# Kernel optimization log

Measured on AMD Instinct MI355X. Metric: run time of the kernel, lower is better.

## Reference

```python
import jax, jax.numpy as jnp
import numpy as np
from jax import lax

NTAG = 31
HID = 100
NEG = -10000.0


def gru_dir(x, w_ih, w_hh, b_ih, b_hh):
    # x: [T, B, 100]; PyTorch gate order in weights: [r, z, n]
    B = x.shape[1]
    h0 = jnp.zeros((B, HID), dtype=x.dtype)

    def step(h, xt):
        gi = xt @ w_ih.T + b_ih          # [B, 3H]
        gh = h @ w_hh.T + b_hh           # [B, 3H]
        ir, iz, inn = jnp.split(gi, 3, axis=-1)
        hr, hz, hn = jnp.split(gh, 3, axis=-1)
        r = jax.nn.sigmoid(ir + hr)
        z = jax.nn.sigmoid(iz + hz)
        n = jnp.tanh(inn + r * hn)
        h = (1.0 - z) * n + z * h
        return h, h

    _, ys = lax.scan(step, h0, x)
    return ys                             # [T, B, H]


def viterbi(feats, msk, transitions):
    # feats: [T, 31], msk: [T], transitions[next, prev]
    init = jnp.full((NTAG,), NEG, dtype=feats.dtype).at[0].set(0.0)
    idx = jnp.arange(NTAG)

    def step(fv, inp):
        feat, m = inp
        scores = fv[None, :] + transitions       # [next, prev]
        bp = jnp.argmax(scores, axis=1)          # [31]
        vv = jnp.max(scores, axis=1) + feat      # [31]
        live = m > 0
        fv_new = jnp.where(live, vv, fv)
        bp = jnp.where(live, bp, idx)            # masked step: identity backpointer
        return fv_new, bp

    fv, bps = lax.scan(step, init, (feats, msk))
    final = jnp.argmax(fv)
    score = fv[final]

    def back(tag, bp):
        return bp[tag], tag

    _, path = lax.scan(back, final, bps, reverse=True)  # path[t] = tag at step t
    return score, path


def setup_inputs() -> dict:
    key = jax.random.key(0)
    ks = jax.random.split(key, 12)
    T, B, D = 2048, 128, 100
    s = 0.1  # ~ 1/sqrt(hidden)
    u = lambda k, sh: jax.random.uniform(k, sh, jnp.float32, -s, s)
    tr = jax.random.normal(ks[10], (NTAG, NTAG), jnp.float32)
    tr = tr.at[0, :].set(NEG).at[:, 29].set(NEG).at[:, 30].set(NEG)
    tr = tr.at[30, 30].set(0.0).at[29, 30].set(0.0)
    return {
        "sentence": jax.random.normal(ks[0], (T, B, D), jnp.float32),
        "mask": jnp.ones((B, T), jnp.float32),
        "w_ih_f": u(ks[1], (3 * HID, D)), "w_hh_f": u(ks[2], (3 * HID, HID)),
        "b_ih_f": u(ks[3], (3 * HID,)), "b_hh_f": u(ks[4], (3 * HID,)),
        "w_ih_b": u(ks[5], (3 * HID, D)), "w_hh_b": u(ks[6], (3 * HID, HID)),
        "b_ih_b": u(ks[7], (3 * HID,)), "b_hh_b": u(ks[8], (3 * HID,)),
        "w_out": u(ks[9], (NTAG, 2 * HID)), "b_out": jnp.zeros((NTAG,), jnp.float32),
        "transitions": tr,
        "batch": B,
        "seq": 0,
    }


def reference(sentence, mask, w_ih_f, w_hh_f, b_ih_f, b_hh_f,
              w_ih_b, w_hh_b, b_ih_b, b_hh_b, w_out, b_out,
              transitions, batch, seq):
    fwd = gru_dir(sentence, w_ih_f, w_hh_f, b_ih_f, b_hh_f)
    bwd = gru_dir(sentence[::-1], w_ih_b, w_hh_b, b_ih_b, b_hh_b)[::-1]
    gru_out = jnp.concatenate([fwd, bwd], axis=-1)        # [T, B, 200]
    feats = gru_out @ w_out.T + b_out                      # [T, B, 31]
    feats_b = jnp.transpose(feats, (1, 0, 2))              # [B, T, 31]
    score, path = viterbi(feats_b[seq], mask[seq], transitions)
    return score, path
```

## Files before the change

### kernel.cpp

```cpp
#include <hip/hip_runtime.h>
#include <stdint.h>

#define TT 2048
#define BB 128
#define DD 100
#define HH 100
#define GG 300
#define NT 31
#define NEGV (-10000.0f)

#define REP25(M) M(0) M(1) M(2) M(3) M(4) M(5) M(6) M(7) M(8) M(9) M(10) M(11) \
                 M(12) M(13) M(14) M(15) M(16) M(17) M(18) M(19) M(20) M(21) M(22) M(23) M(24)
#define REP31(M) M(0) M(1) M(2) M(3) M(4) M(5) M(6) M(7) M(8) M(9) M(10) M(11) \
                 M(12) M(13) M(14) M(15) M(16) M(17) M(18) M(19) M(20) M(21) M(22) M(23) \
                 M(24) M(25) M(26) M(27) M(28) M(29) M(30)
#define REP8(M)  M(0) M(1) M(2) M(3) M(4) M(5) M(6) M(7)

#define RL(v, k) __int_as_float(__builtin_amdgcn_readlane(__float_as_int(v), (k)))

__global__ __launch_bounds__(320) void gi_kernel(
    const float* __restrict__ sent, const int* __restrict__ seqp,
    const float* __restrict__ w_ih_f, const float* __restrict__ b_ih_f,
    const float* __restrict__ w_ih_b, const float* __restrict__ b_ih_b,
    float* __restrict__ gi)
{
    const int t   = blockIdx.x;
    const int dir = blockIdx.y;
    const int j   = threadIdx.x;
    const int seq = seqp[0];
    const int ts  = dir ? (TT - 1 - t) : t;
    __shared__ __align__(16) float x_s[DD];
    if (j < DD) x_s[j] = sent[((size_t)ts * BB + seq) * DD + j];
    __syncthreads();
    if (j < GG) {
        const float* w = dir ? w_ih_b : w_ih_f;
        const float* b = dir ? b_ih_b : b_ih_f;
        const float4* w4 = (const float4*)(w + j * DD);
        const float4* x4 = (const float4*)x_s;
        float a0 = 0.f, a1 = 0.f, a2 = 0.f, a3 = 0.f;
        #pragma unroll
        for (int k = 0; k < DD / 4; k++) {
            float4 wv = w4[k], xv = x4[k];
            a0 += wv.x * xv.x; a1 += wv.y * xv.y;
            a2 += wv.z * xv.z; a3 += wv.w * xv.w;
        }
        gi[((size_t)dir * TT + t) * GG + j] = b[j] + (a0 + a1) + (a2 + a3);
    }
}

__global__ __launch_bounds__(512, 2) void gru_seq_kernel(
    const float* __restrict__ gi,
    const float* __restrict__ w_hh_f, const float* __restrict__ b_hh_f,
    const float* __restrict__ w_hh_b, const float* __restrict__ b_hh_b,
    const float* __restrict__ w_out,
    float* __restrict__ pfeat)
{
    const int dir  = blockIdx.x;
    const int tid  = threadIdx.x;
    const int wave = tid >> 6, lane = tid & 63;
    const int q    = wave >> 1;
    const bool isA = !(wave & 1);
    const int k0   = q * 25;
    const float* w_hh = dir ? w_hh_b : w_hh_f;
    const float* b_hh = dir ? b_hh_b : b_hh_f;
    const float* gid  = gi + (size_t)dir * TT * GG;
    float* pf = pfeat + (size_t)dir * TT * NT;

    __shared__ float part[2][4][384];

    const int s0 = (isA ? 0 : 64) + lane;
    const int s1 = (isA ? 128 : 192) + lane;
    const int s2 = (isA ? 256 : 320) + lane;

    const float* r0 = w_hh + s0 * DD + k0;
    const float* r1 = w_hh + s1 * DD + k0;
    const int wrow = (s2 - GG) < (NT - 1) ? (s2 - GG) : (NT - 1);
    const float* r2 = (s2 < GG) ? (w_hh + s2 * DD + k0)
                                : (w_out + wrow * (2 * HH) + dir * HH + k0);

    #define DECLW(i) float w0_##i, w1_##i, w2_##i;
    REP25(DECLW)
    #define LDW(i) w0_##i = r0[i]; w1_##i = r1[i]; w2_##i = r2[i];
    REP25(LDW)

    const int r = k0 + lane;
    float bhr = 0.f, bhz = 0.f, bhn = 0.f;
    if (lane < 25) { bhr = b_hh[r]; bhz = b_hh[HH + r]; bhn = b_hh[2 * HH + r]; }

    const int  p     = lane - 32;
    const bool is_pf = (wave == 1) && (p >= 0) && (p < NT);
    #define DECLPH(i) float ph##i = 0.f;
    REP8(DECLPH)

    float hreg = 0.f;

    float gAr = 0.f, gAz = 0.f, gAn = 0.f, gBr = 0.f, gBz = 0.f, gBn = 0.f;
    if (lane < 25) {
        gAr = gid[r];      gAz = gid[HH + r];      gAn = gid[2 * HH + r];
        gBr = gid[GG + r]; gBz = gid[GG + HH + r]; gBn = gid[GG + 2 * HH + r];
    }

    #define DOTK(i) { float hk = RL(hreg, i);              \
        a0 = fmaf(hk, w0_##i, a0);                          \
        a1 = fmaf(hk, w1_##i, a1);                          \
        a2 = fmaf(hk, w2_##i, a2); }

    #define GRU_STEP(TIDX, BUF, SLOT, cr, cz, cn) {                          \
        float a0 = 0.f, a1 = 0.f, a2 = 0.f;                                  \
        REP25(DOTK)                                                          \
        part[BUF][q][s0] = a0;                                               \
        part[BUF][q][s1] = a1;                                               \
        part[BUF][q][s2] = a2;                                               \
        __syncthreads();                                                     \
        if (lane < 25) {                                                     \
            float pr = part[BUF][0][r] + part[BUF][1][r]                     \
                     + part[BUF][2][r] + part[BUF][3][r];                    \
            float pz = part[BUF][0][HH + r] + part[BUF][1][HH + r]           \
                     + part[BUF][2][HH + r] + part[BUF][3][HH + r];          \
            float pn = part[BUF][0][2 * HH + r] + part[BUF][1][2 * HH + r]   \
                     + part[BUF][2][2 * HH + r] + part[BUF][3][2 * HH + r];  \
            float xr  = pr + bhr + (cr);                                     \
            float xz  = pz + bhz + (cz);                                     \
            float ghn = pn + bhn;                                            \
            float rr  = 1.f / (1.f + __expf(-xr));                           \
            float zz  = 1.f / (1.f + __expf(-xz));                           \
            float pre = (cn) + rr * ghn;                                     \
            pre = fmaxf(fminf(pre, 40.f), -40.f);                            \
            float e2  = __expf(-2.f * pre);                                  \
            float nn  = (1.f - e2) / (1.f + e2);                             \
            hreg = (1.f - zz) * nn + zz * hreg;                              \
            int tp = (TIDX) + 2; tp = (tp < TT) ? tp : (TT - 1);             \
            cr = gid[tp * GG + r];                                           \
            cz = gid[tp * GG + HH + r];                                      \
            cn = gid[tp * GG + 2 * HH + r];                                  \
        }                                                                    \
        if (is_pf && (TIDX) > 0) {                                           \
            ph##SLOT = part[BUF][0][GG + p] + part[BUF][1][GG + p]           \
                     + part[BUF][2][GG + p] + part[BUF][3][GG + p];          \
        }                                                                    \
    }

    #define PHST(i) pf[(size_t)(dir ? (TT - 1 - (tb + i)) : (tb + i)) * NT + p] = ph##i;

    for (int tt = 0; tt < TT; tt += 8) {
        GRU_STEP(tt + 0, 0, 7, gAr, gAz, gAn)
        if (is_pf && tt >= 8) { int tb = tt - 8; REP8(PHST) }
        GRU_STEP(tt + 1, 1, 0, gBr, gBz, gBn)
        GRU_STEP(tt + 2, 0, 1, gAr, gAz, gAn)
        GRU_STEP(tt + 3, 1, 2, gBr, gBz, gBn)
        GRU_STEP(tt + 4, 0, 3, gAr, gAz, gAn)
        GRU_STEP(tt + 5, 1, 4, gBr, gBz, gBn)
        GRU_STEP(tt + 6, 0, 5, gAr, gAz, gAn)
        GRU_STEP(tt + 7, 1, 6, gBr, gBz, gBn)
    }

    {
        float a2 = 0.f;
        #define DOT2K(i) a2 = fmaf(RL(hreg, i), w2_##i, a2);
        REP25(DOT2K)
        part[0][q][s2] = a2;
        __syncthreads();
        if (is_pf) {
            ph7 = part[0][0][GG + p] + part[0][1][GG + p]
                + part[0][2][GG + p] + part[0][3][GG + p];
            int tb = TT - 8;
            REP8(PHST)
        }
    }
}

__global__ __launch_bounds__(64) void vit_scan_kernel(
    const float* __restrict__ pfeat, const float* __restrict__ mask,
    const int* __restrict__ seqp, const float* __restrict__ trans,
    const float* __restrict__ b_out,
    float* __restrict__ fvg, int* __restrict__ meta, float* __restrict__ out)
{
    const int lane = threadIdx.x;
    const int ln   = (lane < NT) ? lane : (NT - 1);
    const float* mrow = mask + (size_t)seqp[0] * TT;
    const float* pff = pfeat;
    const float* pfb = pfeat + (size_t)TT * NT;

    #define DECLTR(i) float tr##i = trans[ln * NT + i];
    REP31(DECLTR)
    const float bo = b_out[ln];

    float fv = (lane == 0) ? 0.f : NEGV;
    fvg[lane] = fv;

    float ffr[8], fbr[8], mr[8];
    #pragma unroll
    for (int q = 0; q < 8; q++) {
        ffr[q] = pff[q * NT + ln]; fbr[q] = pfb[q * NT + ln]; mr[q] = mrow[q];
    }

    for (int t = 0; t < TT; t += 8) {
        #pragma unroll
        for (int q = 0; q < 8; q++) {
            float fcur = ffr[q] + fbr[q] + bo;
            float mcur = mr[q];
            int tp = t + q + 8; tp = (tp < TT) ? tp : (TT - 1);
            ffr[q] = pff[tp * NT + ln]; fbr[q] = pfb[tp * NT + ln]; mr[q] = mrow[tp];
            #define VADD(i) float v##i = RL(fv, i) + tr##i;
            REP31(VADD)
            #undef VADD
            v0  = fmaxf(v0,  v16); v1  = fmaxf(v1,  v17); v2  = fmaxf(v2,  v18);
            v3  = fmaxf(v3,  v19); v4  = fmaxf(v4,  v20); v5  = fmaxf(v5,  v21);
            v6  = fmaxf(v6,  v22); v7  = fmaxf(v7,  v23); v8  = fmaxf(v8,  v24);
            v9  = fmaxf(v9,  v25); v10 = fmaxf(v10, v26); v11 = fmaxf(v11, v27);
            v12 = fmaxf(v12, v28); v13 = fmaxf(v13, v29); v14 = fmaxf(v14, v30);
            v0 = fmaxf(v0, v8);  v1 = fmaxf(v1, v9);  v2 = fmaxf(v2, v10);
            v3 = fmaxf(v3, v11); v4 = fmaxf(v4, v12); v5 = fmaxf(v5, v13);
            v6 = fmaxf(v6, v14); v7 = fmaxf(v7, v15);
            v0 = fmaxf(v0, v4); v1 = fmaxf(v1, v5); v2 = fmaxf(v2, v6); v3 = fmaxf(v3, v7);
            v0 = fmaxf(v0, v2); v1 = fmaxf(v1, v3);
            float m = fmaxf(v0, v1);
            float cand = m + fcur;
            fv = (mcur > 0.f) ? cand : fv;
            fvg[(t + q + 1) * 64 + lane] = fv;
        }
    }

    float fbest = RL(fv, 0);
    int ftag = 0;
    #pragma unroll
    for (int q = 1; q < NT; q++) {
        float s = RL(fv, q);
        if (s > fbest) { fbest = s; ftag = q; }
    }
    if (lane == 0) { out[0] = fbest; meta[0] = ftag; }
}

__global__ __launch_bounds__(1024) void vit_bp_kernel(
    const float* __restrict__ fvg, const float* __restrict__ mask,
    const int* __restrict__ seqp, const float* __restrict__ trans,
    uint8_t* __restrict__ bpg, uint8_t* __restrict__ gmapg)
{
    const int b    = blockIdx.x;
    const int tid  = threadIdx.x;
    const int wave = tid >> 6, lane = tid & 63;
    const int j    = lane & 31;
    const int jr   = (j < NT) ? j : (NT - 1);
    const float* mrow = mask + (size_t)seqp[0] * TT;

    __shared__ int bpl[64][32];

    float trj[NT];
    #pragma unroll
    for (int q = 0; q < NT; q++) trj[q] = trans[jr * NT + q];

    #pragma unroll
    for (int q4 = 0; q4 < 4; q4++) {
        const int t = b * 64 + wave * 4 + q4;
        float fvp = fvg[t * 64 + lane];
        float mcur = mrow[t];
        float best = RL(fvp, 0) + trj[0];
        int bi = 0;
        #pragma unroll
        for (int q = 1; q < NT; q++) {
            float s = RL(fvp, q) + trj[q];
            if (s > best) { best = s; bi = q; }
        }
        int bpn = (mcur > 0.f) ? bi : j;
        if (j == 31) bpn = 31;
        if (lane < 32) {
            bpl[wave * 4 + q4][lane] = bpn;
            if (j < NT) bpg[(size_t)t * NT + j] = (uint8_t)bpn;
        }
    }
    __syncthreads();
    if (wave == 0) {
        int G = j;
        for (int i = 0; i < 64; i++) {
            int bpv = bpl[i][j];
            G = __shfl(G, bpv);
        }
        if (lane < 32) gmapg[b * 32 + lane] = (uint8_t)G;
    }
}

__global__ __launch_bounds__(64) void vit_back_kernel(
    const uint8_t* __restrict__ bpg, const uint8_t* __restrict__ gmapg,
    const int* __restrict__ meta, float* __restrict__ out)
{
    const int tid = threadIdx.x;
    __shared__ uint8_t bps[TT * NT];
    __shared__ uint8_t gm[32 * 32];
    __shared__ uint8_t echk[32];

    const uint32_t* src = (const uint32_t*)bpg;
    uint32_t* dst = (uint32_t*)bps;
    for (int i = tid; i < TT * NT / 4; i += 64) dst[i] = src[i];
    for (int i = tid; i < 1024 / 4; i += 64)
        ((uint32_t*)gm)[i] = ((const uint32_t*)gmapg)[i];
    __syncthreads();

    if (tid == 0) {
        int tag = meta[0];
        for (int b = 31; b >= 0; b--) { echk[b] = (uint8_t)tag; tag = gm[b * 32 + tag]; }
    }
    __syncthreads();
    if (tid < 32) {
        int tag = echk[tid];
        for (int i = 63; i >= 0; i--) {
            int t = tid * 64 + i;
            out[1 + t] = (float)tag;
            tag = bps[t * NT + tag];
        }
    }
}

extern "C" void kernel_launch(void* const* d_in, const int* in_sizes, int n_in,
                              void* d_out, int out_size, void* d_ws, size_t ws_size,
                              hipStream_t stream) {
    const float* sent   = (const float*)d_in[0];
    const float* mask   = (const float*)d_in[1];
    const float* w_ih_f = (const float*)d_in[2];
    const float* w_hh_f = (const float*)d_in[3];
    const float* b_ih_f = (const float*)d_in[4];
    const float* b_hh_f = (const float*)d_in[5];
    const float* w_ih_b = (const float*)d_in[6];
    const float* w_hh_b = (const float*)d_in[7];
    const float* b_ih_b = (const float*)d_in[8];
    const float* b_hh_b = (const float*)d_in[9];
    const float* w_out  = (const float*)d_in[10];
    const float* b_out  = (const float*)d_in[11];
    const float* trans  = (const float*)d_in[12];
    const int*   seqp   = (const int*)d_in[14];
    float* out = (float*)d_out;

    float* gi    = (float*)d_ws;
    float* pfeat = gi + (size_t)2 * TT * GG;
    float* fvg   = pfeat + (size_t)2 * TT * NT;
    float* bpf   = fvg + (size_t)(TT + 1) * 64;
    uint8_t* bpg   = (uint8_t*)bpf;
    uint8_t* gmapg = bpg + (size_t)TT * NT;
    int*     meta  = (int*)(gmapg + 1024);

    gi_kernel<<<dim3(TT, 2), 320, 0, stream>>>(sent, seqp, w_ih_f, b_ih_f,
                                               w_ih_b, b_ih_b, gi);
    gru_seq_kernel<<<2, 512, 0, stream>>>(gi, w_hh_f, b_hh_f, w_hh_b, b_hh_b,
                                          w_out, pfeat);
    vit_scan_kernel<<<1, 64, 0, stream>>>(pfeat, mask, seqp, trans, b_out,
                                          fvg, meta, out);
    vit_bp_kernel<<<32, 1024, 0, stream>>>(fvg, mask, seqp, trans, bpg, gmapg);
    vit_back_kernel<<<1, 64, 0, stream>>>(bpg, gmapg, meta, out);
}
```

Baseline: 2.193 ms.

## Halve GRU recurrence block to 4 waves using packed FP32 FMA

The sequential GRU kernel drops from 8 waves to 4. Each lane now owns two adjacent gate rows, held as float2 weight pairs and accumulated with v_pk_fma_f32 against a broadcast scalar of h. The aim is to cut barrier cost and wave count per step on the latency-bound recurrence while keeping the number of FMA instructions roughly the same. The Viterbi max reduction is also rewritten as a tree of three-input fmax operations, which could map to v_max3. The risks are higher register pressure from the doubled weights per lane and the constraints of inline asm with a 64-bit SGPR operand.

```diff
diff --git a/kernel.cpp b/kernel.cpp
--- a/kernel.cpp
+++ b/kernel.cpp
@@ -17,6 +17,8 @@
 #define REP8(M)  M(0) M(1) M(2) M(3) M(4) M(5) M(6) M(7)
 
 #define RL(v, k) __int_as_float(__builtin_amdgcn_readlane(__float_as_int(v), (k)))
+
+typedef float f2 __attribute__((ext_vector_type(2)));
 
 __global__ __launch_bounds__(320) void gi_kernel(
     const float* __restrict__ sent, const int* __restrict__ seqp,
@@ -48,7 +50,7 @@
     }
 }
 
-__global__ __launch_bounds__(512, 2) void gru_seq_kernel(
+__global__ __launch_bounds__(256, 1) void gru_seq_kernel(
     const float* __restrict__ gi,
     const float* __restrict__ w_hh_f, const float* __restrict__ b_hh_f,
     const float* __restrict__ w_hh_b, const float* __restrict__ b_hh_b,
@@ -58,29 +60,31 @@
     const int dir  = blockIdx.x;
     const int tid  = threadIdx.x;
     const int wave = tid >> 6, lane = tid & 63;
-    const int q    = wave >> 1;
-    const bool isA = !(wave & 1);
+    const int q    = wave;
     const int k0   = q * 25;
     const float* w_hh = dir ? w_hh_b : w_hh_f;
     const float* b_hh = dir ? b_hh_b : b_hh_f;
     const float* gid  = gi + (size_t)dir * TT * GG;
     float* pf = pfeat + (size_t)dir * TT * NT;
 
-    __shared__ float part[2][4][384];
-
-    const int s0 = (isA ? 0 : 64) + lane;
-    const int s1 = (isA ? 128 : 192) + lane;
-    const int s2 = (isA ? 256 : 320) + lane;
-
-    const float* r0 = w_hh + s0 * DD + k0;
-    const float* r1 = w_hh + s1 * DD + k0;
-    const int wrow = (s2 - GG) < (NT - 1) ? (s2 - GG) : (NT - 1);
-    const float* r2 = (s2 < GG) ? (w_hh + s2 * DD + k0)
-                                : (w_out + wrow * (2 * HH) + dir * HH + k0);
-
-    #define DECLW(i) float w0_##i, w1_##i, w2_##i;
+    __shared__ __align__(16) float part[2][4][384];
+
+    const int P0 = lane, P1 = 64 + lane, P2 = 128 + lane;
+
+    auto rowp = [&](int s) -> const float* {
+        if (s < GG) return w_hh + (size_t)s * DD + k0;
+        int wr = s - GG; if (wr > NT - 1) wr = NT - 1;
+        return w_out + (size_t)wr * (2 * HH) + dir * HH + k0;
+    };
+    const float* a0p = rowp(2 * P0);     const float* b0p = rowp(2 * P0 + 1);
+    const float* a1p = rowp(2 * P1);     const float* b1p = rowp(2 * P1 + 1);
+    const float* a2p = rowp(2 * P2);     const float* b2p = rowp(2 * P2 + 1);
+
+    #define DECLW(i) f2 w0_##i, w1_##i, w2_##i;
     REP25(DECLW)
-    #define LDW(i) w0_##i = r0[i]; w1_##i = r1[i]; w2_##i = r2[i];
+    #define LDW(i) w0_##i.x = a0p[i]; w0_##i.y = b0p[i]; \
+                   w1_##i.x = a1p[i]; w1_##i.y = b1p[i]; \
+                   w2_##i.x = a2p[i]; w2_##i.y = b2p[i];
     REP25(LDW)
 
     const int r = k0 + lane;
@@ -100,17 +104,20 @@
         gBr = gid[GG + r]; gBz = gid[GG + HH + r]; gBn = gid[GG + 2 * HH + r];
     }
 
-    #define DOTK(i) { float hk = RL(hreg, i);              \
-        a0 = fmaf(hk, w0_##i, a0);                          \
-        a1 = fmaf(hk, w1_##i, a1);                          \
-        a2 = fmaf(hk, w2_##i, a2); }
+    #define PKFMA(ACC, W) asm("v_pk_fma_f32 %0, %1, %2, %0" \
+                              : "+v"(ACC) : "v"(W), "s"(hp));
+
+    #define DOTK(i) { unsigned hu = (unsigned)__builtin_amdgcn_readlane(        \
+                          __float_as_int(hreg), (i));                           \
+        uint64_t hp = ((uint64_t)hu << 32) | (uint64_t)hu;                      \
+        PKFMA(acc0, w0_##i) PKFMA(acc1, w1_##i) PKFMA(acc2, w2_##i) }
 
     #define GRU_STEP(TIDX, BUF, SLOT, cr, cz, cn) {                          \
-        float a0 = 0.f, a1 = 0.f, a2 = 0.f;                                  \
+        f2 acc0 = {0.f, 0.f}, acc1 = {0.f, 0.f}, acc2 = {0.f, 0.f};          \
         REP25(DOTK)                                                          \
-        part[BUF][q][s0] = a0;                                               \
-        part[BUF][q][s1] = a1;                                               \
-        part[BUF][q][s2] = a2;                                               \
+        *(f2*)&part[BUF][q][2 * P0] = acc0;                                  \
+        *(f2*)&part[BUF][q][2 * P1] = acc1;                                  \
+        *(f2*)&part[BUF][q][2 * P2] = acc2;                                  \
         __syncthreads();                                                     \
         if (lane < 25) {                                                     \
             float pr = part[BUF][0][r] + part[BUF][1][r]                     \
@@ -155,10 +162,13 @@
     }
 
     {
-        float a2 = 0.f;
-        #define DOT2K(i) a2 = fmaf(RL(hreg, i), w2_##i, a2);
+        f2 acc2e = {0.f, 0.f};
+        #define DOT2K(i) { unsigned hu = (unsigned)__builtin_amdgcn_readlane(   \
+                              __float_as_int(hreg), (i));                       \
+            uint64_t hp = ((uint64_t)hu << 32) | (uint64_t)hu;                  \
+            PKFMA(acc2e, w2_##i) }
         REP25(DOT2K)
-        part[0][q][s2] = a2;
+        *(f2*)&part[0][q][2 * P2] = acc2e;
         __syncthreads();
         if (is_pf) {
             ph7 = part[0][0][GG + p] + part[0][1][GG + p]
@@ -204,17 +214,20 @@
             #define VADD(i) float v##i = RL(fv, i) + tr##i;
             REP31(VADD)
             #undef VADD
-            v0  = fmaxf(v0,  v16); v1  = fmaxf(v1,  v17); v2  = fmaxf(v2,  v18);
-            v3  = fmaxf(v3,  v19); v4  = fmaxf(v4,  v20); v5  = fmaxf(v5,  v21);
-            v6  = fmaxf(v6,  v22); v7  = fmaxf(v7,  v23); v8  = fmaxf(v8,  v24);
-            v9  = fmaxf(v9,  v25); v10 = fmaxf(v10, v26); v11 = fmaxf(v11, v27);
-            v12 = fmaxf(v12, v28); v13 = fmaxf(v13, v29); v14 = fmaxf(v14, v30);
-            v0 = fmaxf(v0, v8);  v1 = fmaxf(v1, v9);  v2 = fmaxf(v2, v10);
-            v3 = fmaxf(v3, v11); v4 = fmaxf(v4, v12); v5 = fmaxf(v5, v13);
-            v6 = fmaxf(v6, v14); v7 = fmaxf(v7, v15);
-            v0 = fmaxf(v0, v4); v1 = fmaxf(v1, v5); v2 = fmaxf(v2, v6); v3 = fmaxf(v3, v7);
-            v0 = fmaxf(v0, v2); v1 = fmaxf(v1, v3);
-            float m = fmaxf(v0, v1);
+            float m0 = fmaxf(fmaxf(v0,  v1),  v2);
+            float m1 = fmaxf(fmaxf(v3,  v4),  v5);
+            float m2 = fmaxf(fmaxf(v6,  v7),  v8);
+            float m3 = fmaxf(fmaxf(v9,  v10), v11);
+            float m4 = fmaxf(fmaxf(v12, v13), v14);
+            float m5 = fmaxf(fmaxf(v15, v16), v17);
+            float m6 = fmaxf(fmaxf(v18, v19), v20);
+            float m7 = fmaxf(fmaxf(v21, v22), v23);
+            float m8 = fmaxf(fmaxf(v24, v25), v26);
+            float m9 = fmaxf(fmaxf(v27, v28), v29);
+            float n0 = fmaxf(fmaxf(m0, m1), m2);
+            float n1 = fmaxf(fmaxf(m3, m4), m5);
+            float n2 = fmaxf(fmaxf(m6, m7), m8);
+            float m  = fmaxf(fmaxf(fmaxf(fmaxf(n0, n1), n2), m9), v30);
             float cand = m + fcur;
             fv = (mcur > 0.f) ? cand : fv;
             fvg[(t + q + 1) * 64 + lane] = fv;
@@ -339,7 +352,7 @@
 
     gi_kernel<<<dim3(TT, 2), 320, 0, stream>>>(sent, seqp, w_ih_f, b_ih_f,
                                                w_ih_b, b_ih_b, gi);
-    gru_seq_kernel<<<2, 512, 0, stream>>>(gi, w_hh_f, b_hh_f, w_hh_b, b_hh_b,
+    gru_seq_kernel<<<2, 256, 0, stream>>>(gi, w_hh_f, b_hh_f, w_hh_b, b_hh_b,
                                           w_out, pfeat);
     vit_scan_kernel<<<1, 64, 0, stream>>>(pfeat, mask, seqp, trans, b_out,
                                           fvg, meta, out);
```

Result: faster. 2.130 ms (-2.9%).
